# Kernel tuning notes

Hardware: AMD Instinct MI355X
Metric: run time of the kernel (lower is better)

Reference implementation:

```python
import jax, jax.numpy as jnp
import numpy as np

N, M, D = 4096, 65536, 256

def setup_inputs() -> dict:
    key = jax.random.key(0)
    k1, k2 = jax.random.split(key)
    x = jax.random.normal(k1, (N, D), dtype=jnp.float32)
    target_set = jax.random.normal(k2, (M, D), dtype=jnp.float32)  # [M, D] database
    return {"x": x, "target_set": target_set}

def reference(x, target_set):
    # L2 metric branch of NNDistance.
    # target_set_norm_squared: [1, M] precomputed at init in the original module.
    t_norm_sq = jnp.sum(target_set * target_set, axis=1)[None, :]  # [1, M]
    x_norm_sq = jnp.sum(x * x, axis=1, keepdims=True)              # [N, 1]
    d2 = x_norm_sq + t_norm_sq - 2.0 * jnp.matmul(x, target_set.T)  # [N, M]
    dists = jnp.sqrt(jnp.maximum(d2, 0.0))
    # torch.min(dists, dim=1) returns (values, indices)
    values = jnp.min(dists, axis=1)
    indices = jnp.argmin(dists, axis=1)
    return values, indices
```

## Files before the change

### kernel.cpp

```cpp
#include <hip/hip_runtime.h>
#include <float.h>
#include <math.h>

#define N_ROWS 4096
#define M_TGT  65536
#define DDIM   256

typedef short bf16x8 __attribute__((ext_vector_type(8)));
typedef float f32x4 __attribute__((ext_vector_type(4)));
typedef unsigned short ushort4_t __attribute__((ext_vector_type(4)));

__device__ inline unsigned short f2bf(float f) {
  union { float f; unsigned u; } c; c.f = f;
  unsigned u = c.u;
  unsigned r = (u + 0x7FFFu + ((u >> 16) & 1u)) >> 16;
  return (unsigned short)r;
}

__device__ inline void gload_lds16(const void* g, void* l) {
  __builtin_amdgcn_global_load_lds(
      (const __attribute__((address_space(1))) void*)g,
      (__attribute__((address_space(3))) void*)l, 16, 0, 0);
}

#define MFMA16(a, b, c) __builtin_amdgcn_mfma_f32_16x16x32_bf16(a, b, c, 0, 0, 0)

__global__ __launch_bounds__(256) void conv_norm_all(
    const float* __restrict__ x, const float* __restrict__ t,
    unsigned short* __restrict__ xb, unsigned short* __restrict__ tb,
    float* __restrict__ xn, float* __restrict__ tn) {
  int wave = threadIdx.x >> 6;
  int lane = threadIdx.x & 63;
  int row  = blockIdx.x * 4 + wave;
  const float* src;
  unsigned short* db;
  float* dn;
  if (row < N_ROWS) {
    src = x + (size_t)row * DDIM;
    db  = xb + (size_t)row * DDIM;
    dn  = xn + row;
  } else {
    int r = row - N_ROWS;
    if (r >= M_TGT) return;
    src = t + (size_t)r * DDIM;
    db  = tb + (size_t)r * DDIM;
    dn  = tn + r;
  }
  float4 v = *(const float4*)(src + lane * 4);
  float ss = v.x * v.x + v.y * v.y + v.z * v.z + v.w * v.w;
  ushort4_t o;
  o[0] = f2bf(v.x); o[1] = f2bf(v.y); o[2] = f2bf(v.z); o[3] = f2bf(v.w);
  *(ushort4_t*)(db + lane * 4) = o;
  #pragma unroll
  for (int off = 32; off > 0; off >>= 1) ss += __shfl_xor(ss, off, 64);
  if (lane == 0) *dn = ss;
}

#define GBM 128
#define GBN 128
#define GBK 64
#define NCB 512
#define NGRP 2048
#define MARGIN 1.5f

__global__ __launch_bounds__(256) void nn_gemm_bf16(
    const unsigned short* __restrict__ xb, const unsigned short* __restrict__ tb,
    const float* __restrict__ tn, float* __restrict__ bmv32) {
  __shared__ __align__(16) unsigned short sX[GBM * GBK];
  __shared__ __align__(16) unsigned short sT[GBN * GBK];
  __shared__ float smin[4][128];

  const int tid  = threadIdx.x;
  const int lane = tid & 63;
  const int wid  = tid >> 6;
  const int wt   = wid >> 1;
  const int wx   = wid & 1;
  const int ln   = lane & 15;
  const int cg   = lane >> 4;

  const int bid = blockIdx.x;
  const int xcd = bid & 7;
  const int wgi = bid >> 3;
  const int rb  = wgi & 31;
  const int cb  = xcd * 64 + (wgi >> 5);
  const int row0 = rb * GBM;
  const int col0 = cb * GBN;

  int rq[4], sq[4];
  #pragma unroll
  for (int i = 0; i < 4; ++i) {
    int q = i * 256 + tid;
    rq[i] = q >> 3;
    sq[i] = (q & 7) ^ (rq[i] & 7);
  }
  char* sXc = (char*)sX;
  char* sTc = (char*)sT;

  f32x4 acc[4][4];
  const f32x4 zero = {0.0f, 0.0f, 0.0f, 0.0f};
  #pragma unroll
  for (int m = 0; m < 4; ++m)
    #pragma unroll
    for (int n = 0; n < 4; ++n) acc[m][n] = zero;

  #pragma unroll
  for (int kc = 0; kc < DDIM; kc += GBK) {
    __syncthreads();
    #pragma unroll
    for (int i = 0; i < 4; ++i)
      gload_lds16(xb + (size_t)(row0 + rq[i]) * DDIM + kc + sq[i] * 8,
                  sXc + i * 4096 + wid * 1024);
    #pragma unroll
    for (int i = 0; i < 4; ++i)
      gload_lds16(tb + (size_t)(col0 + rq[i]) * DDIM + kc + sq[i] * 8,
                  sTc + i * 4096 + wid * 1024);
    __syncthreads();

    bf16x8 tf[4][2], xf[4][2];
    #pragma unroll
    for (int m = 0; m < 4; ++m) {
      int r = wt * 64 + m * 16 + ln;
      #pragma unroll
      for (int kk = 0; kk < 2; ++kk) {
        int p = (kk * 4 + cg) ^ (r & 7);
        tf[m][kk] = *(const bf16x8*)(sTc + r * 128 + p * 16);
      }
    }
    #pragma unroll
    for (int n = 0; n < 4; ++n) {
      int r = wx * 64 + n * 16 + ln;
      #pragma unroll
      for (int kk = 0; kk < 2; ++kk) {
        int p = (kk * 4 + cg) ^ (r & 7);
        xf[n][kk] = *(const bf16x8*)(sXc + r * 128 + p * 16);
      }
    }
    #pragma unroll
    for (int kk = 0; kk < 2; ++kk)
      #pragma unroll
      for (int m = 0; m < 4; ++m)
        #pragma unroll
        for (int n = 0; n < 4; ++n)
          acc[m][n] = MFMA16(tf[m][kk], xf[n][kk], acc[m][n]);
  }

  float tnc[4][4];
  #pragma unroll
  for (int m = 0; m < 4; ++m)
    #pragma unroll
    for (int j = 0; j < 4; ++j)
      tnc[m][j] = tn[col0 + wt * 64 + m * 16 + cg * 4 + j];

  float vres[2][4];
  #pragma unroll
  for (int mh2 = 0; mh2 < 2; ++mh2) {
    #pragma unroll
    for (int n = 0; n < 4; ++n) {
      float v = FLT_MAX;
      #pragma unroll
      for (int mi = 0; mi < 2; ++mi) {
        int m = mh2 * 2 + mi;
        #pragma unroll
        for (int j = 0; j < 4; ++j)
          v = fminf(v, fmaf(-2.0f, acc[m][n][j], tnc[m][j]));
      }
      v = fminf(v, __shfl_xor(v, 16, 64));
      v = fminf(v, __shfl_xor(v, 32, 64));
      vres[mh2][n] = v;
    }
  }

  __syncthreads();
  if (cg == 0) {
    #pragma unroll
    for (int mh2 = 0; mh2 < 2; ++mh2)
      #pragma unroll
      for (int n = 0; n < 4; ++n)
        smin[wt * 2 + mh2][wx * 64 + n * 16 + ln] = vres[mh2][n];
  }
  __syncthreads();
  if (tid < 128) {
    float4 o;
    o.x = smin[0][tid]; o.y = smin[1][tid];
    o.z = smin[2][tid]; o.w = smin[3][tid];
    *(float4*)&bmv32[(size_t)(row0 + tid) * NGRP + (size_t)cb * 4] = o;
  }
}

__global__ __launch_bounds__(256) void nn_exact_fine(
    const float* __restrict__ x, const float* __restrict__ t,
    const float* __restrict__ xn, const float* __restrict__ tn,
    const float* __restrict__ bmv32, float* __restrict__ out) {
  __shared__ float wmin[4];
  __shared__ int   clist[NGRP];
  __shared__ int   cnt;
  __shared__ float rv[256];
  __shared__ int   ri[256];

  const int row = blockIdx.x;
  const int tid = threadIdx.x;
  const float* brow = bmv32 + (size_t)row * NGRP;

  if (tid == 0) cnt = 0;
  float4 v0 = *(const float4*)(brow + tid * 8);
  float4 v1 = *(const float4*)(brow + tid * 8 + 4);
  float lmin = fminf(fminf(fminf(v0.x, v0.y), fminf(v0.z, v0.w)),
                     fminf(fminf(v1.x, v1.y), fminf(v1.z, v1.w)));
  #pragma unroll
  for (int off = 32; off > 0; off >>= 1)
    lmin = fminf(lmin, __shfl_xor(lmin, off, 64));
  if ((tid & 63) == 0) wmin[tid >> 6] = lmin;
  __syncthreads();
  const float thr =
      fminf(fminf(wmin[0], wmin[1]), fminf(wmin[2], wmin[3])) + MARGIN;

  {
    float vv[8] = {v0.x, v0.y, v0.z, v0.w, v1.x, v1.y, v1.z, v1.w};
    #pragma unroll
    for (int k = 0; k < 8; ++k) {
      if (vv[k] <= thr) {
        int p = atomicAdd(&cnt, 1);
        clist[p] = tid * 8 + k;
      }
    }
  }
  __syncthreads();
  const int nc = cnt;

  float best = FLT_MAX;
  int   bidx = 0x7FFFFFFF;
  const float xnr = xn[row];
  const float* xrow = x + (size_t)row * DDIM;

  for (int ci = 0; ci < nc; ci += 8) {
    int slot = ci + (tid >> 5);
    if (slot < nc) {
      int col = clist[slot] * 32 + (tid & 31);
      const float* trow = t + (size_t)col * DDIM;
      float acc = 0.0f;
      for (int kq = 0; kq < DDIM; kq += 4) {
        float4 xv = *(const float4*)(xrow + kq);
        float4 tv = *(const float4*)(trow + kq);
        acc = fmaf(xv.x, tv.x, acc);
        acc = fmaf(xv.y, tv.y, acc);
        acc = fmaf(xv.z, tv.z, acc);
        acc = fmaf(xv.w, tv.w, acc);
      }
      float d2 = xnr + tn[col] - 2.0f * acc;
      if (d2 < best || (d2 == best && col < bidx)) { best = d2; bidx = col; }
    }
  }
  rv[tid] = best; ri[tid] = bidx;
  __syncthreads();
  for (int s = 128; s >= 1; s >>= 1) {
    if (tid < s) {
      float vo = rv[tid + s]; int io = ri[tid + s];
      if (vo < rv[tid] || (vo == rv[tid] && io < ri[tid])) { rv[tid] = vo; ri[tid] = io; }
    }
    __syncthreads();
  }
  if (tid == 0) {
    out[row] = sqrtf(fmaxf(rv[0], 0.0f));
    out[N_ROWS + row] = (float)ri[0];
  }
}

__global__ __launch_bounds__(256) void nn_gemm_mid(
    const unsigned short* __restrict__ xb, const unsigned short* __restrict__ tb,
    const float* __restrict__ tn, float* __restrict__ bmv) {
  __shared__ __align__(16) unsigned short sX[GBM * GBK];
  __shared__ __align__(16) unsigned short sT[GBN * GBK];
  __shared__ float smin[2][128];

  const int tid  = threadIdx.x;
  const int lane = tid & 63;
  const int wid  = tid >> 6;
  const int wt   = wid >> 1;
  const int wx   = wid & 1;
  const int ln   = lane & 15;
  const int cg   = lane >> 4;

  const int bid = blockIdx.x;
  const int xcd = bid & 7;
  const int wgi = bid >> 3;
  const int rb  = wgi & 31;
  const int cb  = xcd * 64 + (wgi >> 5);
  const int row0 = rb * GBM;
  const int col0 = cb * GBN;

  int rq[4], sq[4];
  #pragma unroll
  for (int i = 0; i < 4; ++i) {
    int q = i * 256 + tid;
    rq[i] = q >> 3;
    sq[i] = (q & 7) ^ (rq[i] & 7);
  }
  char* sXc = (char*)sX;
  char* sTc = (char*)sT;

  f32x4 acc[4][4];
  const f32x4 zero = {0.0f, 0.0f, 0.0f, 0.0f};
  #pragma unroll
  for (int m = 0; m < 4; ++m)
    #pragma unroll
    for (int n = 0; n < 4; ++n) acc[m][n] = zero;

  #pragma unroll
  for (int kc = 0; kc < DDIM; kc += GBK) {
    __syncthreads();
    #pragma unroll
    for (int i = 0; i < 4; ++i)
      gload_lds16(xb + (size_t)(row0 + rq[i]) * DDIM + kc + sq[i] * 8,
                  sXc + i * 4096 + wid * 1024);
    #pragma unroll
    for (int i = 0; i < 4; ++i)
      gload_lds16(tb + (size_t)(col0 + rq[i]) * DDIM + kc + sq[i] * 8,
                  sTc + i * 4096 + wid * 1024);
    __syncthreads();

    bf16x8 tf[4][2], xf[4][2];
    #pragma unroll
    for (int m = 0; m < 4; ++m) {
      int r = wt * 64 + m * 16 + ln;
      #pragma unroll
      for (int kk = 0; kk < 2; ++kk) {
        int p = (kk * 4 + cg) ^ (r & 7);
        tf[m][kk] = *(const bf16x8*)(sTc + r * 128 + p * 16);
      }
    }
    #pragma unroll
    for (int n = 0; n < 4; ++n) {
      int r = wx * 64 + n * 16 + ln;
      #pragma unroll
      for (int kk = 0; kk < 2; ++kk) {
        int p = (kk * 4 + cg) ^ (r & 7);
        xf[n][kk] = *(const bf16x8*)(sXc + r * 128 + p * 16);
      }
    }
    #pragma unroll
    for (int kk = 0; kk < 2; ++kk)
      #pragma unroll
      for (int m = 0; m < 4; ++m)
        #pragma unroll
        for (int n = 0; n < 4; ++n)
          acc[m][n] = MFMA16(tf[m][kk], xf[n][kk], acc[m][n]);
  }

  float tnc[4][4];
  #pragma unroll
  for (int m = 0; m < 4; ++m)
    #pragma unroll
    for (int j = 0; j < 4; ++j)
      tnc[m][j] = tn[col0 + wt * 64 + m * 16 + cg * 4 + j];

  float res[4];
  #pragma unroll
  for (int n = 0; n < 4; ++n) {
    float v = FLT_MAX;
    #pragma unroll
    for (int m = 0; m < 4; ++m)
      #pragma unroll
      for (int j = 0; j < 4; ++j)
        v = fminf(v, fmaf(-2.0f, acc[m][n][j], tnc[m][j]));
    v = fminf(v, __shfl_xor(v, 16, 64));
    v = fminf(v, __shfl_xor(v, 32, 64));
    res[n] = v;
  }

  __syncthreads();
  if (cg == 0) {
    #pragma unroll
    for (int n = 0; n < 4; ++n)
      smin[wt][wx * 64 + n * 16 + ln] = res[n];
  }
  __syncthreads();
  if (tid < 128)
    bmv[(size_t)(row0 + tid) * NCB + cb] = fminf(smin[0][tid], smin[1][tid]);
}

__global__ __launch_bounds__(256) void nn_exact_mid(
    const float* __restrict__ x, const float* __restrict__ t,
    const float* __restrict__ xn, const float* __restrict__ tn,
    const float* __restrict__ bmv, float* __restrict__ out) {
  __shared__ float sv[NCB];
  __shared__ int   clist[NCB];
  __shared__ int   cnt;
  __shared__ float wmin[4];
  __shared__ float rv[256];
  __shared__ int   ri[256];

  const int row = blockIdx.x;
  const int tid = threadIdx.x;

  if (tid == 0) cnt = 0;
  float lmin = FLT_MAX;
  #pragma unroll
  for (int e = tid; e < NCB; e += 256) {
    float v = bmv[(size_t)row * NCB + e];
    sv[e] = v;
    lmin = fminf(lmin, v);
  }
  #pragma unroll
  for (int off = 32; off > 0; off >>= 1) lmin = fminf(lmin, __shfl_xor(lmin, off, 64));
  if ((tid & 63) == 0) wmin[tid >> 6] = lmin;
  __syncthreads();
  const float g = fminf(fminf(wmin[0], wmin[1]), fminf(wmin[2], wmin[3]));

  #pragma unroll
  for (int e = tid; e < NCB; e += 256) {
    if (sv[e] <= g + MARGIN) {
      int p = atomicAdd(&cnt, 1);
      clist[p] = e;
    }
  }
  __syncthreads();
  const int nc = cnt;

  float best = FLT_MAX;
  int   bidx = 0x7FFFFFFF;
  const float xnr = xn[row];
  const float* xrow = x + (size_t)row * DDIM;

  for (int ci = 0; ci < nc; ci += 2) {
    int slot = ci + (tid >> 7);
    if (slot < nc) {
      int col = clist[slot] * 128 + (tid & 127);
      const float* trow = t + (size_t)col * DDIM;
      float acc = 0.0f;
      for (int kq = 0; kq < DDIM; kq += 4) {
        float4 xv = *(const float4*)(xrow + kq);
        float4 tv = *(const float4*)(trow + kq);
        acc = fmaf(xv.x, tv.x, acc);
        acc = fmaf(xv.y, tv.y, acc);
        acc = fmaf(xv.z, tv.z, acc);
        acc = fmaf(xv.w, tv.w, acc);
      }
      float d2 = xnr + tn[col] - 2.0f * acc;
      if (d2 < best || (d2 == best && col < bidx)) { best = d2; bidx = col; }
    }
  }
  rv[tid] = best; ri[tid] = bidx;
  __syncthreads();
  for (int s = 128; s >= 1; s >>= 1) {
    if (tid < s) {
      float vo = rv[tid + s]; int io = ri[tid + s];
      if (vo < rv[tid] || (vo == rv[tid] && io < ri[tid])) { rv[tid] = vo; ri[tid] = io; }
    }
    __syncthreads();
  }
  if (tid == 0) {
    out[row] = sqrtf(fmaxf(rv[0], 0.0f));
    out[N_ROWS + row] = (float)ri[0];
  }
}

#define BM 64
#define BN 64
#define KC 16
#define S_STRIPS 32
#define PADM 68

__global__ __launch_bounds__(256) void norms_kernel_fb(
    const float* __restrict__ x, const float* __restrict__ t,
    float* __restrict__ xn, float* __restrict__ tn) {
  int wave = threadIdx.x >> 6;
  int lane = threadIdx.x & 63;
  int row  = blockIdx.x * 4 + wave;
  const float* src; float* dst;
  if (row < N_ROWS) { src = x + (size_t)row * DDIM; dst = xn + row; }
  else {
    int r = row - N_ROWS;
    if (r >= M_TGT) return;
    src = t + (size_t)r * DDIM; dst = tn + r;
  }
  float4 v = *(const float4*)(src + lane * 4);
  float s = v.x * v.x + v.y * v.y + v.z * v.z + v.w * v.w;
  #pragma unroll
  for (int off = 32; off > 0; off >>= 1) s += __shfl_xor(s, off, 64);
  if (lane == 0) *dst = s;
}

__global__ __launch_bounds__(256) void nn_main_fb(
    const float* __restrict__ x, const float* __restrict__ t,
    const float* __restrict__ xn, const float* __restrict__ tn,
    float* __restrict__ pmin, int* __restrict__ pidx) {
  __shared__ float sx[KC][PADM];
  __shared__ float st[KC][PADM];
  const int tid = threadIdx.x;
  const int rb = blockIdx.x;
  const int strip = blockIdx.y;
  const int tx = tid & 15, ty = tid >> 4;
  const int row0 = rb * BM;
  const int col_start = strip * (M_TGT / S_STRIPS);
  const int ntiles = (M_TGT / S_STRIPS) / BN;
  const int srow = tid >> 2;
  const int kq = (tid & 3) * 4;

  float runMin[4]; int runIdx[4];
  #pragma unroll
  for (int r = 0; r < 4; ++r) { runMin[r] = FLT_MAX; runIdx[r] = 0; }
  float xnr[4];
  #pragma unroll
  for (int r = 0; r < 4; ++r) xnr[r] = xn[row0 + ty * 4 + r];

  for (int tile = 0; tile < ntiles; ++tile) {
    const int cbk = col_start + tile * BN;
    float acc[4][4];
    #pragma unroll
    for (int r = 0; r < 4; ++r)
      #pragma unroll
      for (int c = 0; c < 4; ++c) acc[r][c] = 0.0f;
    #pragma unroll 1
    for (int kc = 0; kc < DDIM; kc += KC) {
      float4 xv = *(const float4*)(x + (size_t)(row0 + srow) * DDIM + kc + kq);
      float4 tv = *(const float4*)(t + (size_t)(cbk + srow) * DDIM + kc + kq);
      __syncthreads();
      sx[kq + 0][srow] = xv.x; sx[kq + 1][srow] = xv.y;
      sx[kq + 2][srow] = xv.z; sx[kq + 3][srow] = xv.w;
      st[kq + 0][srow] = tv.x; st[kq + 1][srow] = tv.y;
      st[kq + 2][srow] = tv.z; st[kq + 3][srow] = tv.w;
      __syncthreads();
      #pragma unroll
      for (int k = 0; k < KC; ++k) {
        float4 xa = *(const float4*)&sx[k][ty * 4];
        float4 tb2 = *(const float4*)&st[k][tx * 4];
        float xr[4] = {xa.x, xa.y, xa.z, xa.w};
        float tc[4] = {tb2.x, tb2.y, tb2.z, tb2.w};
        #pragma unroll
        for (int r = 0; r < 4; ++r)
          #pragma unroll
          for (int c = 0; c < 4; ++c)
            acc[r][c] = fmaf(xr[r], tc[c], acc[r][c]);
      }
    }
    #pragma unroll
    for (int r = 0; r < 4; ++r)
      #pragma unroll
      for (int c = 0; c < 4; ++c) {
        int col = cbk + tx * 4 + c;
        float d2 = xnr[r] + tn[col] - 2.0f * acc[r][c];
        if (d2 < runMin[r]) { runMin[r] = d2; runIdx[r] = col; }
      }
  }
  __syncthreads();
  float* redv = &sx[0][0];
  int*   redi = (int*)&st[0][0];
  #pragma unroll
  for (int r = 0; r < 4; ++r) {
    int lrow = ty * 4 + r;
    redv[lrow * 16 + tx] = runMin[r];
    redi[lrow * 16 + tx] = runIdx[r];
  }
  __syncthreads();
  if (tid < 64) {
    float best = FLT_MAX; int bi = 0;
    #pragma unroll
    for (int j = 0; j < 16; ++j) {
      float v = redv[tid * 16 + j];
      int   i = redi[tid * 16 + j];
      if (v < best || (v == best && i < bi)) { best = v; bi = i; }
    }
    int grow = row0 + tid;
    pmin[(size_t)grow * S_STRIPS + strip] = best;
    pidx[(size_t)grow * S_STRIPS + strip] = bi;
  }
}

__global__ __launch_bounds__(256) void reduce_final_fb(
    const float* __restrict__ pmin, const int* __restrict__ pidx,
    float* __restrict__ out) {
  int row = blockIdx.x * 256 + threadIdx.x;
  if (row >= N_ROWS) return;
  float best = FLT_MAX; int bi = 0;
  #pragma unroll 4
  for (int s = 0; s < S_STRIPS; ++s) {
    float v = pmin[(size_t)row * S_STRIPS + s];
    int   i = pidx[(size_t)row * S_STRIPS + s];
    if (v < best || (v == best && i < bi)) { best = v; bi = i; }
  }
  out[row] = sqrtf(fmaxf(best, 0.0f));
  out[N_ROWS + row] = (float)bi;
}

extern "C" void kernel_launch(void* const* d_in, const int* in_sizes, int n_in,
                              void* d_out, int out_size, void* d_ws, size_t ws_size,
                              hipStream_t stream) {
  const float* x = (const float*)d_in[0];
  const float* t = (const float*)d_in[1];
  float* ws = (float*)d_ws;
  float* out = (float*)d_out;

  float* xn = ws;
  float* tn = ws + N_ROWS;

  const size_t f_bmvF = (size_t)N_ROWS + M_TGT;
  const size_t f_xbF  = f_bmvF + (size_t)N_ROWS * NGRP;
  const size_t f_tbF  = f_xbF + ((size_t)N_ROWS * DDIM) / 2;
  const size_t need_fine = (f_tbF + ((size_t)M_TGT * DDIM) / 2) * sizeof(float);

  const size_t f_bmvM = (size_t)N_ROWS + M_TGT;
  const size_t f_xbM  = f_bmvM + (size_t)N_ROWS * NCB;
  const size_t f_tbM  = f_xbM + ((size_t)N_ROWS * DDIM) / 2;
  const size_t need_mid = (f_tbM + ((size_t)M_TGT * DDIM) / 2) * sizeof(float);

  if (ws_size >= need_fine) {
    float* bmv32 = ws + f_bmvF;
    unsigned short* xb = (unsigned short*)(ws + f_xbF);
    unsigned short* tb = (unsigned short*)(ws + f_tbF);

    conv_norm_all<<<(N_ROWS + M_TGT) / 4, 256, 0, stream>>>(x, t, xb, tb, xn, tn);
    nn_gemm_bf16<<<(N_ROWS / GBM) * NCB, 256, 0, stream>>>(xb, tb, tn, bmv32);
    nn_exact_fine<<<N_ROWS, 256, 0, stream>>>(x, t, xn, tn, bmv32, out);
  } else if (ws_size >= need_mid) {
    float* bmv = ws + f_bmvM;
    unsigned short* xb = (unsigned short*)(ws + f_xbM);
    unsigned short* tb = (unsigned short*)(ws + f_tbM);

    conv_norm_all<<<(N_ROWS + M_TGT) / 4, 256, 0, stream>>>(x, t, xb, tb, xn, tn);
    nn_gemm_mid<<<(N_ROWS / GBM) * NCB, 256, 0, stream>>>(xb, tb, tn, bmv);
    nn_exact_mid<<<N_ROWS, 256, 0, stream>>>(x, t, xn, tn, bmv, out);
  } else {
    norms_kernel_fb<<<(N_ROWS + M_TGT) / 4, 256, 0, stream>>>(x, t, xn, tn);
    float* pmin = ws + N_ROWS + M_TGT;
    int*   pidx = (int*)(ws + N_ROWS + M_TGT + (size_t)N_ROWS * S_STRIPS);
    dim3 grid(N_ROWS / BM, S_STRIPS);
    nn_main_fb<<<grid, 256, 0, stream>>>(x, t, xn, tn, pmin, pidx);
    reduce_final_fb<<<(N_ROWS + 255) / 256, 256, 0, stream>>>(pmin, pidx, out);
  }
}
```

Baseline: 201.3 us.

## Widen fine GEMM tile to 128x256 with 512-thread blocks

Doubles the target-column tile of the bf16 distance GEMM to 256 and the block to 8 waves, so each staged X tile is reused across twice as many target columns and the grid halves. Staging loads are re-indexed for 512 threads, and the per-block min output now writes 8 group minima per row. This cuts redundant X loads and launch overhead, at the cost of more LDS per block and possibly lower occupancy. The mid-path kernel keeps its old 128x128 tile through new macros.

After: 190.7 us, median of 2. 5.3% less time.

```diff
diff --git a/kernel.cpp b/kernel.cpp
--- a/kernel.cpp
+++ b/kernel.cpp
@@ -57,18 +57,18 @@
 }
 
 #define GBM 128
-#define GBN 128
+#define GBN2 256
 #define GBK 64
 #define NCB 512
 #define NGRP 2048
 #define MARGIN 1.5f
 
-__global__ __launch_bounds__(256) void nn_gemm_bf16(
+__global__ __launch_bounds__(512) void nn_gemm_bf16(
     const unsigned short* __restrict__ xb, const unsigned short* __restrict__ tb,
     const float* __restrict__ tn, float* __restrict__ bmv32) {
   __shared__ __align__(16) unsigned short sX[GBM * GBK];
-  __shared__ __align__(16) unsigned short sT[GBN * GBK];
-  __shared__ float smin[4][128];
+  __shared__ __align__(16) unsigned short sT[GBN2 * GBK];
+  __shared__ float smin[8][128];
 
   const int tid  = threadIdx.x;
   const int lane = tid & 63;
@@ -80,18 +80,25 @@
 
   const int bid = blockIdx.x;
   const int xcd = bid & 7;
-  const int wgi = bid >> 3;
-  const int rb  = wgi & 31;
-  const int cb  = xcd * 64 + (wgi >> 5);
+  const int w   = bid >> 3;
+  const int rb  = w & 31;
+  const int cb  = xcd * 32 + (w >> 5);
   const int row0 = rb * GBM;
-  const int col0 = cb * GBN;
-
-  int rq[4], sq[4];
+  const int col0 = cb * GBN2;
+
+  int rqa[2], sqa[2];
+  #pragma unroll
+  for (int i = 0; i < 2; ++i) {
+    int q = i * 512 + tid;
+    rqa[i] = q >> 3;
+    sqa[i] = (q & 7) ^ (rqa[i] & 7);
+  }
+  int rqb[4], sqb[4];
   #pragma unroll
   for (int i = 0; i < 4; ++i) {
-    int q = i * 256 + tid;
-    rq[i] = q >> 3;
-    sq[i] = (q & 7) ^ (rq[i] & 7);
+    int q = i * 512 + tid;
+    rqb[i] = q >> 3;
+    sqb[i] = (q & 7) ^ (rqb[i] & 7);
   }
   char* sXc = (char*)sX;
   char* sTc = (char*)sT;
@@ -107,13 +114,13 @@
   for (int kc = 0; kc < DDIM; kc += GBK) {
     __syncthreads();
     #pragma unroll
+    for (int i = 0; i < 2; ++i)
+      gload_lds16(xb + (size_t)(row0 + rqa[i]) * DDIM + kc + sqa[i] * 8,
+                  sXc + (i * 512 + tid) * 16);
+    #pragma unroll
     for (int i = 0; i < 4; ++i)
-      gload_lds16(xb + (size_t)(row0 + rq[i]) * DDIM + kc + sq[i] * 8,
-                  sXc + i * 4096 + wid * 1024);
-    #pragma unroll
-    for (int i = 0; i < 4; ++i)
-      gload_lds16(tb + (size_t)(col0 + rq[i]) * DDIM + kc + sq[i] * 8,
-                  sTc + i * 4096 + wid * 1024);
+      gload_lds16(tb + (size_t)(col0 + rqb[i]) * DDIM + kc + sqb[i] * 8,
+                  sTc + (i * 512 + tid) * 16);
     __syncthreads();
 
     bf16x8 tf[4][2], xf[4][2];
@@ -170,7 +177,6 @@
     }
   }
 
-  __syncthreads();
   if (cg == 0) {
     #pragma unroll
     for (int mh2 = 0; mh2 < 2; ++mh2)
@@ -180,10 +186,14 @@
   }
   __syncthreads();
   if (tid < 128) {
-    float4 o;
-    o.x = smin[0][tid]; o.y = smin[1][tid];
-    o.z = smin[2][tid]; o.w = smin[3][tid];
-    *(float4*)&bmv32[(size_t)(row0 + tid) * NGRP + (size_t)cb * 4] = o;
+    float4 o0, o1;
+    o0.x = smin[0][tid]; o0.y = smin[1][tid];
+    o0.z = smin[2][tid]; o0.w = smin[3][tid];
+    o1.x = smin[4][tid]; o1.y = smin[5][tid];
+    o1.z = smin[6][tid]; o1.w = smin[7][tid];
+    float* dst = &bmv32[(size_t)(row0 + tid) * NGRP + (size_t)cb * 8];
+    *(float4*)dst = o0;
+    *(float4*)(dst + 4) = o1;
   }
 }
 
@@ -265,11 +275,14 @@
   }
 }
 
+#define MGBM 128
+#define MGBN 128
+
 __global__ __launch_bounds__(256) void nn_gemm_mid(
     const unsigned short* __restrict__ xb, const unsigned short* __restrict__ tb,
     const float* __restrict__ tn, float* __restrict__ bmv) {
-  __shared__ __align__(16) unsigned short sX[GBM * GBK];
-  __shared__ __align__(16) unsigned short sT[GBN * GBK];
+  __shared__ __align__(16) unsigned short sX[MGBM * GBK];
+  __shared__ __align__(16) unsigned short sT[MGBN * GBK];
   __shared__ float smin[2][128];
 
   const int tid  = threadIdx.x;
@@ -285,8 +298,8 @@
   const int wgi = bid >> 3;
   const int rb  = wgi & 31;
   const int cb  = xcd * 64 + (wgi >> 5);
-  const int row0 = rb * GBM;
-  const int col0 = cb * GBN;
+  const int row0 = rb * MGBM;
+  const int col0 = cb * MGBN;
 
   int rq[4], sq[4];
   #pragma unroll
@@ -609,7 +622,7 @@
     unsigned short* tb = (unsigned short*)(ws + f_tbF);
 
     conv_norm_all<<<(N_ROWS + M_TGT) / 4, 256, 0, stream>>>(x, t, xb, tb, xn, tn);
-    nn_gemm_bf16<<<(N_ROWS / GBM) * NCB, 256, 0, stream>>>(xb, tb, tn, bmv32);
+    nn_gemm_bf16<<<(N_ROWS / GBM) * (M_TGT / GBN2), 512, 0, stream>>>(xb, tb, tn, bmv32);
     nn_exact_fine<<<N_ROWS, 256, 0, stream>>>(x, t, xn, tn, bmv32, out);
   } else if (ws_size >= need_mid) {
     float* bmv = ws + f_bmvM;
@@ -617,7 +630,7 @@
     unsigned short* tb = (unsigned short*)(ws + f_tbM);
 
     conv_norm_all<<<(N_ROWS + M_TGT) / 4, 256, 0, stream>>>(x, t, xb, tb, xn, tn);
-    nn_gemm_mid<<<(N_ROWS / GBM) * NCB, 256, 0, stream>>>(xb, tb, tn, bmv);
+    nn_gemm_mid<<<(N_ROWS / MGBM) * NCB, 256, 0, stream>>>(xb, tb, tn, bmv);
     nn_exact_mid<<<N_ROWS, 256, 0, stream>>>(x, t, xn, tn, bmv, out);
   } else {
     norms_kernel_fb<<<(N_ROWS + M_TGT) / 4, 256, 0, stream>>>(x, t, xn, tn);
```
